# Performance work log

Hardware: AMD Instinct MI355X
Metric: run time of the kernel (lower is better)

## Reference

```python
import jax, jax.numpy as jnp
import numpy as np

G_CRYSTALS = 64   # number of crystals in the batch
N_ATOMS = 64      # atoms per crystal (dense n^2 edge block per crystal)
N_HEADS = 8
HEAD_DIM = 64


def _make_edges(g, n):
    # dense all-pairs (i, j) within each crystal; atoms of crystal c occupy [c*n, (c+1)*n)
    base = np.arange(g, dtype=np.int32)[:, None, None] * n   # (G,1,1)
    idx = np.arange(n, dtype=np.int32)
    e0 = np.broadcast_to(base + idx[None, :, None], (g, n, n)).reshape(-1)  # query index
    e1 = np.broadcast_to(base + idx[None, None, :], (g, n, n)).reshape(-1)  # key index
    return jnp.asarray(np.stack([e0, e1], axis=0))  # (2, M)


def setup_inputs() -> dict:
    key = jax.random.key(0)
    k0, k1, k2, k3, k4 = jax.random.split(key, 5)
    N = G_CRYSTALS * N_ATOMS                 # 4096 atoms total
    M = G_CRYSTALS * N_ATOMS * N_ATOMS       # 262144 edges
    q = jax.random.normal(k0, (N, N_HEADS, HEAD_DIM), jnp.float32)
    k = jax.random.normal(k1, (N, N_HEADS, HEAD_DIM), jnp.float32)
    v = jax.random.normal(k2, (N, N_HEADS, HEAD_DIM), jnp.float32)
    attn_weights = jax.random.normal(k3, (M, N_HEADS), jnp.float32)          # per-edge additive bias
    values = jax.random.normal(k4, (M, N_HEADS, HEAD_DIM), jnp.float32) * 0.1  # per-edge fused value term
    edges = _make_edges(G_CRYSTALS, N_ATOMS)
    return {"q": q, "k": k, "v": v, "attn_weights": attn_weights,
            "values": values, "edges": edges}


def reference(q, k, v, attn_weights, values, edges):
    # Faithful to the norm_func_mode==0 ('default') fallback path of
    # _scaled_dot_product_attention: per-edge logits, softmax over keys per
    # query (within each crystal's dense block), fused value term.
    N, H, Dh = q.shape
    e0, e1 = edges[0], edges[1]
    scale = 1.0 / jnp.sqrt(jnp.asarray(Dh, q.dtype))
    # per-edge attention logits: (M, H)
    a = jnp.einsum('mhd,mhd->mh', q[e0] * scale, k[e1]) + attn_weights
    # stable softmax over edges sharing the same query index e0
    m = jax.ops.segment_max(a, e0, num_segments=N)      # (N, H)
    p = jnp.exp(a - m[e0])                              # (M, H)
    denom = jax.ops.segment_sum(p, e0, num_segments=N)  # (N, H)
    w = p / denom[e0]                                   # (M, H)
    # output[i] = sum_j w[ij] * (v[j] + values[ij])
    out = jax.ops.segment_sum(w[:, :, None] * (v[e1] + values), e0, num_segments=N)
    return out  # (N, H, Dh)
```

## Files before the change

kernel.cpp:

```cpp
#include <hip/hip_runtime.h>


#define NH 8
#define HD 64
#define ROWSTRIDE 68

typedef float f4 __attribute__((ext_vector_type(4)));

__global__ __launch_bounds__(1024, 8)
void crystal_attn_kernel(const float* __restrict__ q,
                         const float* __restrict__ k,
                         const float* __restrict__ v,
                         const float* __restrict__ aw,
                         const float* __restrict__ values,
                         float* __restrict__ out) {
    const int c = blockIdx.x & 63;
    const int h = blockIdx.x >> 6;
    const int t = threadIdx.x;

    __shared__ __align__(16) float sq[64][ROWSTRIDE];
    __shared__ __align__(16) float sk[64][ROWSTRIDE];
    __shared__ __align__(16) float sv[64][ROWSTRIDE];
    __shared__ __align__(16) float sa[64][ROWSTRIDE];
    __shared__ float sden[64];

    {
        const size_t rowbase = ((size_t)c * 64) * (NH * HD) + (size_t)h * HD;
        const float* qg = q + rowbase;
        const float* kg = k + rowbase;
        const float* vg = v + rowbase;
        const int row = t >> 4;
        const int col = (t & 15) * 4;
        const size_t goff = (size_t)row * (NH * HD) + col;
        *(float4*)&sq[row][col] = *(const float4*)(qg + goff);
        *(float4*)&sk[row][col] = *(const float4*)(kg + goff);
        *(float4*)&sv[row][col] = *(const float4*)(vg + goff);

        const float* ag = aw + ((size_t)c * 4096) * NH + h;
        #pragma unroll
        for (int s = 0; s < 4; ++s) {
            int idx = t + 1024 * s;
            sa[idx >> 6][idx & 63] = ag[(size_t)idx * NH];
        }
    }
    __syncthreads();

    {
        const int w = t >> 6;
        const int i = t & 63;
        const int jbase = w * 4;
        float acc[4];
        #pragma unroll
        for (int jj = 0; jj < 4; ++jj) acc[jj] = 0.f;
        #pragma unroll 4
        for (int d4 = 0; d4 < 16; ++d4) {
            float4 qv = *(const float4*)&sq[i][d4 * 4];
            #pragma unroll
            for (int jj = 0; jj < 4; ++jj) {
                float4 kv = *(const float4*)&sk[jbase + jj][d4 * 4];
                acc[jj] += qv.x * kv.x + qv.y * kv.y + qv.z * kv.z + qv.w * kv.w;
            }
        }
        #pragma unroll
        for (int jj = 0; jj < 4; ++jj)
            sa[i][jbase + jj] = acc[jj] * 0.125f + sa[i][jbase + jj];
    }
    __syncthreads();

    {
        const int r  = t >> 4;
        const int jb = (t & 15) * 4;
        float mx = -1e30f;
        #pragma unroll
        for (int jj = 0; jj < 4; ++jj) mx = fmaxf(mx, sa[r][jb + jj]);
        mx = fmaxf(mx, __shfl_xor(mx, 1));
        mx = fmaxf(mx, __shfl_xor(mx, 2));
        mx = fmaxf(mx, __shfl_xor(mx, 4));
        mx = fmaxf(mx, __shfl_xor(mx, 8));
        float sum = 0.f;
        #pragma unroll
        for (int jj = 0; jj < 4; ++jj) {
            float p = __expf(sa[r][jb + jj] - mx);
            sa[r][jb + jj] = p;
            sum += p;
        }
        sum += __shfl_xor(sum, 1);
        sum += __shfl_xor(sum, 2);
        sum += __shfl_xor(sum, 4);
        sum += __shfl_xor(sum, 8);
        if ((t & 15) == 0) sden[r] = sum;
    }
    __syncthreads();

    {
        const int w    = t >> 6;
        const int lane = t & 63;
        const int e    = lane >> 4;
        const int dq   = lane & 15;
        const int i    = 4 * w + e;

        const float* vrow = values
            + ((size_t)(c * 4096 + i * 64)) * (NH * HD)
            + (size_t)h * HD + dq * 4;
        float4 acc = make_float4(0.f, 0.f, 0.f, 0.f);
        #pragma unroll 4
        for (int j = 0; j < 64; ++j) {
            f4 val = __builtin_nontemporal_load(
                         (const f4*)(vrow + (size_t)j * (NH * HD)));
            float  p  = sa[i][j];
            float4 sj = *(const float4*)&sv[j][dq * 4];
            acc.x += p * (sj.x + val.x);
            acc.y += p * (sj.y + val.y);
            acc.z += p * (sj.z + val.z);
            acc.w += p * (sj.w + val.w);
        }
        const float inv = 1.0f / sden[i];
        float* ob = out + ((size_t)(c * 64 + i)) * (NH * HD) + (size_t)h * HD + dq * 4;
        *(float4*)ob = make_float4(acc.x * inv, acc.y * inv, acc.z * inv, acc.w * inv);
    }
}

extern "C" void kernel_launch(void* const* d_in, const int* in_sizes, int n_in,
                              void* d_out, int out_size, void* d_ws, size_t ws_size,
                              hipStream_t stream) {
    const float* q      = (const float*)d_in[0];
    const float* k      = (const float*)d_in[1];
    const float* v      = (const float*)d_in[2];
    const float* aw     = (const float*)d_in[3];
    const float* values = (const float*)d_in[4];
    float* out = (float*)d_out;

    dim3 grid(512);
    dim3 block(1024);
    hipLaunchKernelGGL(crystal_attn_kernel, grid, block, 0, stream,
                       q, k, v, aw, values, out);
}
```

Before: 688.9 us.

## Split attention into weights kernel and values-streaming kernel with coalesced reads

The single fused kernel becomes two. The first computes normalized softmax weights, writes them to a workspace buffer, and accumulates the w·v part into the output. The second kernel handles one crystal and a group of 8 query rows per block across all 8 heads, so each 4 lanes of a row of `values` read a contiguous 2 KB span instead of 256 bytes per head. It then adds the w·values contribution to the output with a read-modify-write. The aim is better coalescing of the dominant `values` stream, at the cost of a second launch, an extra workspace round trip and a reread of the output.

```diff
diff --git a/kernel.cpp b/kernel.cpp
--- a/kernel.cpp
+++ b/kernel.cpp
@@ -8,11 +8,11 @@
 typedef float f4 __attribute__((ext_vector_type(4)));
 
 __global__ __launch_bounds__(1024, 8)
-void crystal_attn_kernel(const float* __restrict__ q,
+void attn_weights_kernel(const float* __restrict__ q,
                          const float* __restrict__ k,
                          const float* __restrict__ v,
                          const float* __restrict__ aw,
-                         const float* __restrict__ values,
+                         float* __restrict__ wbuf,
                          float* __restrict__ out) {
     const int c = blockIdx.x & 63;
     const int h = blockIdx.x >> 6;
@@ -22,19 +22,15 @@
     __shared__ __align__(16) float sk[64][ROWSTRIDE];
     __shared__ __align__(16) float sv[64][ROWSTRIDE];
     __shared__ __align__(16) float sa[64][ROWSTRIDE];
-    __shared__ float sden[64];
 
     {
         const size_t rowbase = ((size_t)c * 64) * (NH * HD) + (size_t)h * HD;
-        const float* qg = q + rowbase;
-        const float* kg = k + rowbase;
-        const float* vg = v + rowbase;
         const int row = t >> 4;
         const int col = (t & 15) * 4;
         const size_t goff = (size_t)row * (NH * HD) + col;
-        *(float4*)&sq[row][col] = *(const float4*)(qg + goff);
-        *(float4*)&sk[row][col] = *(const float4*)(kg + goff);
-        *(float4*)&sv[row][col] = *(const float4*)(vg + goff);
+        *(float4*)&sq[row][col] = *(const float4*)(q + rowbase + goff);
+        *(float4*)&sk[row][col] = *(const float4*)(k + rowbase + goff);
+        *(float4*)&sv[row][col] = *(const float4*)(v + rowbase + goff);
 
         const float* ag = aw + ((size_t)c * 4096) * NH + h;
         #pragma unroll
@@ -70,27 +66,32 @@
     {
         const int r  = t >> 4;
         const int jb = (t & 15) * 4;
-        float mx = -1e30f;
-        #pragma unroll
-        for (int jj = 0; jj < 4; ++jj) mx = fmaxf(mx, sa[r][jb + jj]);
+        float a0 = sa[r][jb + 0], a1 = sa[r][jb + 1];
+        float a2 = sa[r][jb + 2], a3 = sa[r][jb + 3];
+        float mx = fmaxf(fmaxf(a0, a1), fmaxf(a2, a3));
         mx = fmaxf(mx, __shfl_xor(mx, 1));
         mx = fmaxf(mx, __shfl_xor(mx, 2));
         mx = fmaxf(mx, __shfl_xor(mx, 4));
         mx = fmaxf(mx, __shfl_xor(mx, 8));
-        float sum = 0.f;
-        #pragma unroll
-        for (int jj = 0; jj < 4; ++jj) {
-            float p = __expf(sa[r][jb + jj] - mx);
-            sa[r][jb + jj] = p;
-            sum += p;
-        }
+        float p0 = __expf(a0 - mx), p1 = __expf(a1 - mx);
+        float p2 = __expf(a2 - mx), p3 = __expf(a3 - mx);
+        float sum = p0 + p1 + p2 + p3;
         sum += __shfl_xor(sum, 1);
         sum += __shfl_xor(sum, 2);
         sum += __shfl_xor(sum, 4);
         sum += __shfl_xor(sum, 8);
-        if ((t & 15) == 0) sden[r] = sum;
+        const float inv = 1.0f / sum;
+        sa[r][jb + 0] = p0 * inv;
+        sa[r][jb + 1] = p1 * inv;
+        sa[r][jb + 2] = p2 * inv;
+        sa[r][jb + 3] = p3 * inv;
     }
     __syncthreads();
+
+    {
+        float4 wv = *(const float4*)&sa[t >> 4][(t & 15) * 4];
+        *(float4*)(wbuf + (((size_t)c * NH + h) * 4096) + (size_t)t * 4) = wv;
+    }
 
     {
         const int w    = t >> 6;
@@ -98,26 +99,73 @@
         const int e    = lane >> 4;
         const int dq   = lane & 15;
         const int i    = 4 * w + e;
-
-        const float* vrow = values
-            + ((size_t)(c * 4096 + i * 64)) * (NH * HD)
-            + (size_t)h * HD + dq * 4;
         float4 acc = make_float4(0.f, 0.f, 0.f, 0.f);
-        #pragma unroll 4
+        #pragma unroll 8
         for (int j = 0; j < 64; ++j) {
-            f4 val = __builtin_nontemporal_load(
-                         (const f4*)(vrow + (size_t)j * (NH * HD)));
             float  p  = sa[i][j];
             float4 sj = *(const float4*)&sv[j][dq * 4];
-            acc.x += p * (sj.x + val.x);
-            acc.y += p * (sj.y + val.y);
-            acc.z += p * (sj.z + val.z);
-            acc.w += p * (sj.w + val.w);
+            acc.x += p * sj.x;
+            acc.y += p * sj.y;
+            acc.z += p * sj.z;
+            acc.w += p * sj.w;
         }
-        const float inv = 1.0f / sden[i];
         float* ob = out + ((size_t)(c * 64 + i)) * (NH * HD) + (size_t)h * HD + dq * 4;
-        *(float4*)ob = make_float4(acc.x * inv, acc.y * inv, acc.z * inv, acc.w * inv);
+        *(float4*)ob = acc;
     }
+}
+
+__global__ __launch_bounds__(1024, 8)
+void attn_values_kernel(const float* __restrict__ values,
+                        const float* __restrict__ wbuf,
+                        float* __restrict__ out) {
+    const int c  = blockIdx.x >> 3;
+    const int ic = blockIdx.x & 7;
+    const int t  = threadIdx.x;
+
+    __shared__ float sw[8][64][NH + 1];
+
+    {
+        const int h  = t >> 7;
+        const int r  = t & 127;
+        const int il = r >> 4;
+        const int j0 = (r & 15) * 4;
+        const float* src = wbuf + (((size_t)c * NH + h) * 64 + (ic * 8 + il)) * 64 + j0;
+        float4 wv = *(const float4*)src;
+        sw[il][j0 + 0][h] = wv.x;
+        sw[il][j0 + 1][h] = wv.y;
+        sw[il][j0 + 2][h] = wv.z;
+        sw[il][j0 + 3][h] = wv.w;
+    }
+    __syncthreads();
+
+    const int wv_  = t >> 6;
+    const int lane = t & 63;
+    const int il   = wv_ >> 1;
+    const int half = wv_ & 1;
+    const int h    = half * 4 + (lane >> 4);
+    const int dq   = lane & 15;
+    const int i    = ic * 8 + il;
+
+    const float* vrow = values
+        + ((size_t)(c * 4096 + i * 64)) * (NH * HD)
+        + (size_t)h * HD + dq * 4;
+
+    float4 acc = make_float4(0.f, 0.f, 0.f, 0.f);
+    #pragma unroll 8
+    for (int j = 0; j < 64; ++j) {
+        f4 val = __builtin_nontemporal_load(
+                     (const f4*)(vrow + (size_t)j * (NH * HD)));
+        float p = sw[il][j][h];
+        acc.x += p * val.x;
+        acc.y += p * val.y;
+        acc.z += p * val.z;
+        acc.w += p * val.w;
+    }
+
+    float* ob = out + ((size_t)(c * 64 + i)) * (NH * HD) + (size_t)h * HD + dq * 4;
+    float4 o = *(const float4*)ob;
+    o.x += acc.x; o.y += acc.y; o.z += acc.z; o.w += acc.w;
+    *(float4*)ob = o;
 }
 
 extern "C" void kernel_launch(void* const* d_in, const int* in_sizes, int n_in,
@@ -128,10 +176,12 @@
     const float* v      = (const float*)d_in[2];
     const float* aw     = (const float*)d_in[3];
     const float* values = (const float*)d_in[4];
-    float* out = (float*)d_out;
+    float* out  = (float*)d_out;
+    float* wbuf = (float*)d_ws;
 
-    dim3 grid(512);
     dim3 block(1024);
-    hipLaunchKernelGGL(crystal_attn_kernel, grid, block, 0, stream,
-                       q, k, v, aw, values, out);
+    hipLaunchKernelGGL(attn_weights_kernel, dim3(512), block, 0, stream,
+                       q, k, v, aw, wbuf, out);
+    hipLaunchKernelGGL(attn_values_kernel, dim3(512), block, 0, stream,
+                       values, wbuf, out);
 }
```

Measured after the change: 690.3 us. About the same (+0.2%).

## Repartition blocks by query-row chunk across all heads for contiguous values streaming

Applied to the files above, without the earlier changes.

Each block now handles 8 query atoms of one crystal across all 8 heads, instead of all 64 atoms for a single head. The per-edge values tensor and attention bias are therefore read as fully contiguous 16 KB rows, rather than head-strided 256-byte pieces scattered across the whole tensor. The values contribution is reduced across threads through shared memory, with extra barriers per query row. K and V rows are read from global memory repeatedly by several blocks, and softmax normalisation is folded into the weights before the reductions.

```diff
diff --git a/kernel.cpp b/kernel.cpp
--- a/kernel.cpp
+++ b/kernel.cpp
@@ -3,120 +3,142 @@
 
 #define NH 8
 #define HD 64
-#define ROWSTRIDE 68
 
 typedef float f4 __attribute__((ext_vector_type(4)));
 
 __global__ __launch_bounds__(1024, 8)
-void crystal_attn_kernel(const float* __restrict__ q,
-                         const float* __restrict__ k,
-                         const float* __restrict__ v,
-                         const float* __restrict__ aw,
-                         const float* __restrict__ values,
-                         float* __restrict__ out) {
-    const int c = blockIdx.x & 63;
-    const int h = blockIdx.x >> 6;
-    const int t = threadIdx.x;
+void crystal_attn_fused(const float* __restrict__ q,
+                        const float* __restrict__ k,
+                        const float* __restrict__ v,
+                        const float* __restrict__ aw,
+                        const float* __restrict__ values,
+                        float* __restrict__ out) {
+    const int c  = blockIdx.x & 63;
+    const int ic = blockIdx.x >> 6;
+    const int t  = threadIdx.x;
 
-    __shared__ __align__(16) float sq[64][ROWSTRIDE];
-    __shared__ __align__(16) float sk[64][ROWSTRIDE];
-    __shared__ __align__(16) float sv[64][ROWSTRIDE];
-    __shared__ __align__(16) float sa[64][ROWSTRIDE];
-    __shared__ float sden[64];
+    __shared__ __align__(16) float  sq[8][NH * HD];
+    __shared__ __align__(16) float  sa[64][68];
+    __shared__ __align__(16) float4 red[8][128];
+    __shared__ __align__(16) float4 vpart[8][128];
 
     {
-        const size_t rowbase = ((size_t)c * 64) * (NH * HD) + (size_t)h * HD;
-        const float* qg = q + rowbase;
-        const float* kg = k + rowbase;
-        const float* vg = v + rowbase;
-        const int row = t >> 4;
-        const int col = (t & 15) * 4;
-        const size_t goff = (size_t)row * (NH * HD) + col;
-        *(float4*)&sq[row][col] = *(const float4*)(qg + goff);
-        *(float4*)&sk[row][col] = *(const float4*)(kg + goff);
-        *(float4*)&sv[row][col] = *(const float4*)(vg + goff);
-
-        const float* ag = aw + ((size_t)c * 4096) * NH + h;
-        #pragma unroll
-        for (int s = 0; s < 4; ++s) {
-            int idx = t + 1024 * s;
-            sa[idx >> 6][idx & 63] = ag[(size_t)idx * NH];
-        }
+        const float* qg = q + (size_t)(c * 64 + ic * 8) * (NH * HD);
+        const int il = t >> 7, off = (t & 127) * 4;
+        *(float4*)&sq[il][off] = *(const float4*)(qg + (size_t)il * (NH * HD) + off);
+    }
+    {
+        const float* ag = aw + (size_t)(c * 4096 + ic * 512) * NH;
+        float4 a4 = *(const float4*)(ag + (size_t)t * 4);
+        const int ml = t >> 1, h0 = (t & 1) * 4;
+        const int il = ml >> 6, j = ml & 63;
+        sa[il * 8 + h0 + 0][j] = a4.x;
+        sa[il * 8 + h0 + 1][j] = a4.y;
+        sa[il * 8 + h0 + 2][j] = a4.z;
+        sa[il * 8 + h0 + 3][j] = a4.w;
     }
     __syncthreads();
 
     {
-        const int w = t >> 6;
-        const int i = t & 63;
-        const int jbase = w * 4;
-        float acc[4];
-        #pragma unroll
-        for (int jj = 0; jj < 4; ++jj) acc[jj] = 0.f;
+        const int h = t >> 7, j = (t >> 1) & 63, ilh = t & 1;
+        const float* krow = k + ((size_t)(c * 64 + j) * NH + h) * HD;
+        const int r0 = (ilh * 4) * 8 + h;
+        float a0 = 0.f, a1 = 0.f, a2 = 0.f, a3 = 0.f;
         #pragma unroll 4
         for (int d4 = 0; d4 < 16; ++d4) {
-            float4 qv = *(const float4*)&sq[i][d4 * 4];
-            #pragma unroll
-            for (int jj = 0; jj < 4; ++jj) {
-                float4 kv = *(const float4*)&sk[jbase + jj][d4 * 4];
-                acc[jj] += qv.x * kv.x + qv.y * kv.y + qv.z * kv.z + qv.w * kv.w;
-            }
+            float4 kv = *(const float4*)(krow + d4 * 4);
+            float4 q0 = *(const float4*)&sq[ilh * 4 + 0][h * 64 + d4 * 4];
+            float4 q1 = *(const float4*)&sq[ilh * 4 + 1][h * 64 + d4 * 4];
+            float4 q2 = *(const float4*)&sq[ilh * 4 + 2][h * 64 + d4 * 4];
+            float4 q3 = *(const float4*)&sq[ilh * 4 + 3][h * 64 + d4 * 4];
+            a0 += q0.x * kv.x + q0.y * kv.y + q0.z * kv.z + q0.w * kv.w;
+            a1 += q1.x * kv.x + q1.y * kv.y + q1.z * kv.z + q1.w * kv.w;
+            a2 += q2.x * kv.x + q2.y * kv.y + q2.z * kv.z + q2.w * kv.w;
+            a3 += q3.x * kv.x + q3.y * kv.y + q3.z * kv.z + q3.w * kv.w;
         }
-        #pragma unroll
-        for (int jj = 0; jj < 4; ++jj)
-            sa[i][jbase + jj] = acc[jj] * 0.125f + sa[i][jbase + jj];
+        sa[r0 +  0][j] = a0 * 0.125f + sa[r0 +  0][j];
+        sa[r0 +  8][j] = a1 * 0.125f + sa[r0 +  8][j];
+        sa[r0 + 16][j] = a2 * 0.125f + sa[r0 + 16][j];
+        sa[r0 + 24][j] = a3 * 0.125f + sa[r0 + 24][j];
     }
     __syncthreads();
 
     {
         const int r  = t >> 4;
         const int jb = (t & 15) * 4;
-        float mx = -1e30f;
-        #pragma unroll
-        for (int jj = 0; jj < 4; ++jj) mx = fmaxf(mx, sa[r][jb + jj]);
+        float b0 = sa[r][jb + 0], b1 = sa[r][jb + 1];
+        float b2 = sa[r][jb + 2], b3 = sa[r][jb + 3];
+        float mx = fmaxf(fmaxf(b0, b1), fmaxf(b2, b3));
         mx = fmaxf(mx, __shfl_xor(mx, 1));
         mx = fmaxf(mx, __shfl_xor(mx, 2));
         mx = fmaxf(mx, __shfl_xor(mx, 4));
         mx = fmaxf(mx, __shfl_xor(mx, 8));
-        float sum = 0.f;
-        #pragma unroll
-        for (int jj = 0; jj < 4; ++jj) {
-            float p = __expf(sa[r][jb + jj] - mx);
-            sa[r][jb + jj] = p;
-            sum += p;
-        }
+        float p0 = __expf(b0 - mx), p1 = __expf(b1 - mx);
+        float p2 = __expf(b2 - mx), p3 = __expf(b3 - mx);
+        float sum = p0 + p1 + p2 + p3;
         sum += __shfl_xor(sum, 1);
         sum += __shfl_xor(sum, 2);
         sum += __shfl_xor(sum, 4);
         sum += __shfl_xor(sum, 8);
-        if ((t & 15) == 0) sden[r] = sum;
+        const float inv = 1.0f / sum;
+        sa[r][jb + 0] = p0 * inv;
+        sa[r][jb + 1] = p1 * inv;
+        sa[r][jb + 2] = p2 * inv;
+        sa[r][jb + 3] = p3 * inv;
     }
     __syncthreads();
 
     {
-        const int w    = t >> 6;
-        const int lane = t & 63;
-        const int e    = lane >> 4;
-        const int dq   = lane & 15;
-        const int i    = 4 * w + e;
+        const int il = t >> 7, h = (t >> 4) & 7, dq = t & 15;
+        const float* vb = v + ((size_t)(c * 64) * NH + h) * HD + dq * 4;
+        const float* wr = &sa[il * 8 + h][0];
+        float4 acc = make_float4(0.f, 0.f, 0.f, 0.f);
+        #pragma unroll 8
+        for (int j = 0; j < 64; ++j) {
+            float  p  = wr[j];
+            float4 vv = *(const float4*)(vb + (size_t)j * (NH * HD));
+            acc.x += p * vv.x;
+            acc.y += p * vv.y;
+            acc.z += p * vv.z;
+            acc.w += p * vv.w;
+        }
+        vpart[il][t & 127] = *(float4*)&acc;
+    }
 
-        const float* vrow = values
-            + ((size_t)(c * 4096 + i * 64)) * (NH * HD)
-            + (size_t)h * HD + dq * 4;
-        float4 acc = make_float4(0.f, 0.f, 0.f, 0.f);
-        #pragma unroll 4
-        for (int j = 0; j < 64; ++j) {
-            f4 val = __builtin_nontemporal_load(
-                         (const f4*)(vrow + (size_t)j * (NH * HD)));
-            float  p  = sa[i][j];
-            float4 sj = *(const float4*)&sv[j][dq * 4];
-            acc.x += p * (sj.x + val.x);
-            acc.y += p * (sj.y + val.y);
-            acc.z += p * (sj.z + val.z);
-            acc.w += p * (sj.w + val.w);
+    {
+        const float* region = values + (size_t)(c * 4096 + ic * 512) * (NH * HD);
+        const int e = t >> 7;
+        const int h = (t >> 4) & 7;
+        for (int il = 0; il < 8; ++il) {
+            const float* rowp = region + (size_t)il * 64 * (NH * HD) + (size_t)t * 4;
+            const float* wr = &sa[il * 8 + h][0];
+            float4 acc = make_float4(0.f, 0.f, 0.f, 0.f);
+            #pragma unroll
+            for (int chunk = 0; chunk < 8; ++chunk) {
+                f4 val = *(const f4*)(rowp + (size_t)chunk * 4096);
+                float p = wr[chunk * 8 + e];
+                acc.x += p * val.x;
+                acc.y += p * val.y;
+                acc.z += p * val.z;
+                acc.w += p * val.w;
+            }
+            red[e][t & 127] = *(float4*)&acc;
+            __syncthreads();
+            if (t < 128) {
+                float4 s0 = red[0][t], s1 = red[1][t], s2 = red[2][t], s3 = red[3][t];
+                float4 s4 = red[4][t], s5 = red[5][t], s6 = red[6][t], s7 = red[7][t];
+                float4 vp = vpart[il][t];
+                float4 s;
+                s.x = (((s0.x + s1.x) + (s2.x + s3.x)) + ((s4.x + s5.x) + (s6.x + s7.x))) + vp.x;
+                s.y = (((s0.y + s1.y) + (s2.y + s3.y)) + ((s4.y + s5.y) + (s6.y + s7.y))) + vp.y;
+                s.z = (((s0.z + s1.z) + (s2.z + s3.z)) + ((s4.z + s5.z) + (s6.z + s7.z))) + vp.z;
+                s.w = (((s0.w + s1.w) + (s2.w + s3.w)) + ((s4.w + s5.w) + (s6.w + s7.w))) + vp.w;
+                const int hh = t >> 4, dd = t & 15;
+                float* ob = out + ((size_t)(c * 64 + ic * 8 + il) * NH + hh) * HD + dd * 4;
+                *(float4*)ob = s;
+            }
+            __syncthreads();
         }
-        const float inv = 1.0f / sden[i];
-        float* ob = out + ((size_t)(c * 64 + i)) * (NH * HD) + (size_t)h * HD + dq * 4;
-        *(float4*)ob = make_float4(acc.x * inv, acc.y * inv, acc.z * inv, acc.w * inv);
     }
 }
 
@@ -132,6 +154,6 @@
 
     dim3 grid(512);
     dim3 block(1024);
-    hipLaunchKernelGGL(crystal_attn_kernel, grid, block, 0, stream,
+    hipLaunchKernelGGL(crystal_attn_fused, grid, block, 0, stream,
                        q, k, v, aw, values, out);
 }
```

Result: slower. 706.4 us (+2.5%).
